# Kernel tuning notes

Measured on AMD Instinct MI355X. Metric: run time of the kernel, lower is better.

The kernel has to match this reference:

```python
import jax, jax.numpy as jnp
from jax import lax
import numpy as np

B, D = 1_000_000, 20


def setup_inputs() -> dict:
    key = jax.random.key(0)
    kx, kw, kb, ki = jax.random.split(key, 4)
    bound = 1.0 / np.sqrt(D)  # torch nn.Linear init scale
    return {
        "X": jax.random.normal(kx, (B, D), dtype=jnp.float32),
        "W": jax.random.uniform(kw, (D, D), dtype=jnp.float32, minval=-bound, maxval=bound),
        "b": jax.random.uniform(kb, (D,), dtype=jnp.float32, minval=-bound, maxval=bound),
        "W_init": jax.random.normal(ki, (D, D), dtype=jnp.float32),
    }


def reference(X, W, b, W_init):
    # linear -> matmul(+1) -> relu -> same linear again
    h = X @ W.T + b                       # [B, D]
    h = jax.nn.relu(h @ W_init + 1.0)     # [B, D]
    h = h @ W.T + b                       # [B, D]

    # while h.abs().sum() > 1: h /= 2
    # Halving by 2 is exact in fp32, so the abs-sum exactly halves each
    # iteration; count iterations on a scalar, then apply one fused scale.
    s0 = jnp.sum(jnp.abs(h))

    def cond(state):
        s, _ = state
        return s > 1.0

    def body(state):
        s, k = state
        return s * 0.5, k + 1

    _, k = lax.while_loop(cond, body, (s0, jnp.int32(0)))
    scale = jnp.exp2(-k.astype(h.dtype))  # 2**-k, exact for integer k
    return jnp.sum(h * scale)
```

## Files before the change

kernel.cpp:

```cpp
#include <hip/hip_runtime.h>
#include <math.h>

#define D 20
#define ITER 5

typedef __attribute__((ext_vector_type(8))) __bf16 bf16x8;
typedef __attribute__((ext_vector_type(4))) float f32x4;

#define WS_B1_BYTE 0
#define WS_B2_BYTE 2048
#define WS_C_BYTE 4096
#define WS_BB_BYTE 4224
#define WS_PART_BYTE 8192

__device__ __forceinline__ unsigned f2bf_u(float f) {
  unsigned u = __float_as_uint(f);
  u += 0x7fffu + ((u >> 16) & 1u);
  return u >> 16;
}

__global__ void prep_kernel(const float* __restrict__ W,
                            const float* __restrict__ b,
                            const float* __restrict__ Wi,
                            unsigned char* __restrict__ ws) {
  unsigned short* fb1 = (unsigned short*)(ws + WS_B1_BYTE);
  unsigned short* fb2 = (unsigned short*)(ws + WS_B2_BYTE);
  float* cpad = (float*)(ws + WS_C_BYTE);
  float* bpad = (float*)(ws + WS_BB_BYTE);

  const int t = threadIdx.x;
  {
    const int tile = t >> 9, rem = t & 511;
    const int lane = rem >> 3, j = rem & 7;
    const int k = (lane >> 4) * 8 + j;
    const int n = tile * 16 + (lane & 15);
    float v1 = 0.f, v2 = 0.f;
    if (k < D && n < D) {
      float a = 0.f;
#pragma unroll
      for (int e = 0; e < D; ++e) a = fmaf(W[e * D + k], Wi[e * D + n], a);
      v1 = a;
      v2 = W[n * D + k];
    }
    fb1[t] = (unsigned short)f2bf_u(v1);
    fb2[t] = (unsigned short)f2bf_u(v2);
  }
  if (t < 32) {
    float cv = 0.f, bv = 0.f;
    if (t < D) {
      float a = 1.0f;
#pragma unroll
      for (int e = 0; e < D; ++e) a = fmaf(b[e], Wi[e * D + t], a);
      cv = a;
      bv = b[t];
    }
    cpad[t] = cv;
    bpad[t] = bv;
  }
}

__global__ __launch_bounds__(256, 4) void fused_kernel(
    const float* __restrict__ X,
    const unsigned char* __restrict__ ws,
    double* __restrict__ partials) {
  __shared__ __align__(16) float sP[4 * 16 * 36];
  __shared__ float sred[8];

  const uint4* __restrict__ fb1 = (const uint4*)(ws + WS_B1_BYTE);
  const uint4* __restrict__ fb2 = (const uint4*)(ws + WS_B2_BYTE);
  const float* __restrict__ cpad = (const float*)(ws + WS_C_BYTE);
  const float* __restrict__ bpad = (const float*)(ws + WS_BB_BYTE);

  const int t = threadIdx.x;
  const int wave = t >> 6, lane = t & 63;
  const int m = lane & 15, oct = lane >> 4;
  const int k0 = oct * 8;
  const int ko1 = (k0 < D) ? k0 : 0;
  const int ko2 = (k0 + 4 < D) ? k0 + 4 : 0;
  const float s1m = (k0 < D) ? 1.f : 0.f;
  const float s2m = (k0 + 4 < D) ? 1.f : 0.f;

  union UB { bf16x8 v; uint4 q; } b10, b11, b20, b21;
  b10.q = fb1[0 * 64 + lane];
  b11.q = fb1[1 * 64 + lane];
  b20.q = fb2[0 * 64 + lane];
  b21.q = fb2[1 * 64 + lane];
  const float c0 = cpad[m], c1 = cpad[16 + m];
  const float bb0 = bpad[m], bb1 = bpad[16 + m];

  float* wp = sP + wave * 576;
  const float4* rp = (const float4*)(wp + m * 36 + k0);

  const long long wavebase = (long long)blockIdx.x * (4 * ITER * 16) + wave * (ITER * 16);

  float rs = 0.f, ra = 0.f;

  long long rowg = wavebase + m;
  float4 v1 = *(const float4*)(X + rowg * D + ko1);
  float4 v2 = *(const float4*)(X + rowg * D + ko2);

#pragma unroll
  for (int it = 0; it < ITER; ++it) {
    float4 n1, n2;
    if (it + 1 < ITER) {
      const long long rn = wavebase + (it + 1) * 16 + m;
      n1 = *(const float4*)(X + rn * D + ko1);
      n2 = *(const float4*)(X + rn * D + ko2);
    }

    union UF { bf16x8 v; unsigned u[4]; } a1;
    a1.u[0] = f2bf_u(v1.x * s1m) | (f2bf_u(v1.y * s1m) << 16);
    a1.u[1] = f2bf_u(v1.z * s1m) | (f2bf_u(v1.w * s1m) << 16);
    a1.u[2] = f2bf_u(v2.x * s2m) | (f2bf_u(v2.y * s2m) << 16);
    a1.u[3] = f2bf_u(v2.z * s2m) | (f2bf_u(v2.w * s2m) << 16);

    f32x4 acc0 = {c0, c0, c0, c0};
    f32x4 acc1 = {c1, c1, c1, c1};
    acc0 = __builtin_amdgcn_mfma_f32_16x16x32_bf16(a1.v, b10.v, acc0, 0, 0, 0);
    acc1 = __builtin_amdgcn_mfma_f32_16x16x32_bf16(a1.v, b11.v, acc1, 0, 0, 0);

#pragma unroll
    for (int i = 0; i < 4; ++i) {
      wp[(4 * oct + i) * 36 + m] = fmaxf(acc0[i], 0.f);
      wp[(4 * oct + i) * 36 + 16 + m] = fmaxf(acc1[i], 0.f);
    }
    float4 p1 = rp[0], p2 = rp[1];

    union UF a2;
    a2.u[0] = f2bf_u(p1.x) | (f2bf_u(p1.y) << 16);
    a2.u[1] = f2bf_u(p1.z) | (f2bf_u(p1.w) << 16);
    a2.u[2] = f2bf_u(p2.x) | (f2bf_u(p2.y) << 16);
    a2.u[3] = f2bf_u(p2.z) | (f2bf_u(p2.w) << 16);

    f32x4 d0 = {bb0, bb0, bb0, bb0};
    f32x4 d1 = {bb1, bb1, bb1, bb1};
    d0 = __builtin_amdgcn_mfma_f32_16x16x32_bf16(a2.v, b20.v, d0, 0, 0, 0);
    d1 = __builtin_amdgcn_mfma_f32_16x16x32_bf16(a2.v, b21.v, d1, 0, 0, 0);

#pragma unroll
    for (int i = 0; i < 4; ++i) {
      rs += d0[i] + d1[i];
      ra += fabsf(d0[i]) + fabsf(d1[i]);
    }

    if (it + 1 < ITER) {
      v1 = n1;
      v2 = n2;
    }
  }

#pragma unroll
  for (int off = 32; off > 0; off >>= 1) {
    rs += __shfl_down(rs, off, 64);
    ra += __shfl_down(ra, off, 64);
  }
  if (lane == 0) {
    sred[wave] = rs;
    sred[4 + wave] = ra;
  }
  __syncthreads();
  if (t == 0) {
    float s1 = sred[0] + sred[1] + sred[2] + sred[3];
    float s2 = sred[4] + sred[5] + sred[6] + sred[7];
    partials[2 * blockIdx.x + 0] = (double)s1;
    partials[2 * blockIdx.x + 1] = (double)s2;
  }
}

__global__ void fin_kernel(const double* __restrict__ partials,
                           float* __restrict__ out, int nblocks) {
  __shared__ double sredh[16], sreda[16];
  const int t = threadIdx.x;
  double sh = 0.0, sa = 0.0;
  for (int i = t; i < nblocks; i += 1024) {
    sh += partials[2 * i + 0];
    sa += partials[2 * i + 1];
  }
#pragma unroll
  for (int off = 32; off > 0; off >>= 1) {
    sh += __shfl_down(sh, off, 64);
    sa += __shfl_down(sa, off, 64);
  }
  const int wave = t >> 6, lane = t & 63;
  if (lane == 0) {
    sredh[wave] = sh;
    sreda[wave] = sa;
  }
  __syncthreads();
  if (t == 0) {
    double th = 0.0, ta = 0.0;
#pragma unroll
    for (int w = 0; w < 16; ++w) {
      th += sredh[w];
      ta += sreda[w];
    }
    int k = 0;
    while (ta > 1.0 && k < 1100) {
      ta *= 0.5;
      ++k;
    }
    out[0] = ldexpf((float)th, -k);
  }
}

extern "C" void kernel_launch(void* const* d_in, const int* in_sizes, int n_in,
                              void* d_out, int out_size, void* d_ws, size_t ws_size,
                              hipStream_t stream) {
  const float* X = (const float*)d_in[0];
  const float* W = (const float*)d_in[1];
  const float* b = (const float*)d_in[2];
  const float* Wi = (const float*)d_in[3];
  float* out = (float*)d_out;
  unsigned char* ws = (unsigned char*)d_ws;

  const int nrows = in_sizes[0] / D;
  const int nblocks = nrows / (4 * ITER * 16);
  double* partials = (double*)(ws + WS_PART_BYTE);

  hipLaunchKernelGGL(prep_kernel, dim3(1), dim3(1024), 0, stream, W, b, Wi, ws);
  hipLaunchKernelGGL(fused_kernel, dim3(nblocks), dim3(256), 0, stream,
                     X, ws, partials);
  hipLaunchKernelGGL(fin_kernel, dim3(1), dim3(1024), 0, stream, partials, out,
                     nblocks);
}
```

Measured before the change: 119.2 us.

## Fuse final reduction into main kernel via last-block atomic counter; use vector bf16 convert

Removes the separate finalize kernel launch. Each block now bumps an atomic counter after writing its partials, and the last block to finish reduces all partials and computes the output scale. Separately, the manual round-to-nearest bf16 packing is replaced with __builtin_convertvector, which can map to hardware packed conversion, and zero-padding is now done with bitmasks. This saves one launch and its gap, in exchange for a serial tail in the last block and an extra atomic and fence per block.

```diff
diff --git a/kernel.cpp b/kernel.cpp
--- a/kernel.cpp
+++ b/kernel.cpp
@@ -5,12 +5,14 @@
 #define ITER 5
 
 typedef __attribute__((ext_vector_type(8))) __bf16 bf16x8;
+typedef __attribute__((ext_vector_type(8))) float f32x8;
 typedef __attribute__((ext_vector_type(4))) float f32x4;
 
 #define WS_B1_BYTE 0
 #define WS_B2_BYTE 2048
 #define WS_C_BYTE 4096
 #define WS_BB_BYTE 4224
+#define WS_CNT_BYTE 4480
 #define WS_PART_BYTE 8192
 
 __device__ __forceinline__ unsigned f2bf_u(float f) {
@@ -29,6 +31,7 @@
   float* bpad = (float*)(ws + WS_BB_BYTE);
 
   const int t = threadIdx.x;
+  if (t == 0) *(unsigned*)(ws + WS_CNT_BYTE) = 0u;
   {
     const int tile = t >> 9, rem = t & 511;
     const int lane = rem >> 3, j = rem & 7;
@@ -62,9 +65,13 @@
 __global__ __launch_bounds__(256, 4) void fused_kernel(
     const float* __restrict__ X,
     const unsigned char* __restrict__ ws,
-    double* __restrict__ partials) {
+    double* __restrict__ partials,
+    unsigned* __restrict__ cnt,
+    float* __restrict__ out) {
   __shared__ __align__(16) float sP[4 * 16 * 36];
   __shared__ float sred[8];
+  __shared__ double sredh[4], sreda[4];
+  __shared__ int slast;
 
   const uint4* __restrict__ fb1 = (const uint4*)(ws + WS_B1_BYTE);
   const uint4* __restrict__ fb2 = (const uint4*)(ws + WS_B2_BYTE);
@@ -77,8 +84,8 @@
   const int k0 = oct * 8;
   const int ko1 = (k0 < D) ? k0 : 0;
   const int ko2 = (k0 + 4 < D) ? k0 + 4 : 0;
-  const float s1m = (k0 < D) ? 1.f : 0.f;
-  const float s2m = (k0 + 4 < D) ? 1.f : 0.f;
+  const unsigned msk1 = (k0 < D) ? 0xffffffffu : 0u;
+  const unsigned msk2 = (k0 + 4 < D) ? 0xffffffffu : 0u;
 
   union UB { bf16x8 v; uint4 q; } b10, b11, b20, b21;
   b10.q = fb1[0 * 64 + lane];
@@ -109,10 +116,14 @@
     }
 
     union UF { bf16x8 v; unsigned u[4]; } a1;
-    a1.u[0] = f2bf_u(v1.x * s1m) | (f2bf_u(v1.y * s1m) << 16);
-    a1.u[1] = f2bf_u(v1.z * s1m) | (f2bf_u(v1.w * s1m) << 16);
-    a1.u[2] = f2bf_u(v2.x * s2m) | (f2bf_u(v2.y * s2m) << 16);
-    a1.u[3] = f2bf_u(v2.z * s2m) | (f2bf_u(v2.w * s2m) << 16);
+    {
+      f32x8 f1 = {v1.x, v1.y, v1.z, v1.w, v2.x, v2.y, v2.z, v2.w};
+      a1.v = __builtin_convertvector(f1, bf16x8);
+      a1.u[0] &= msk1;
+      a1.u[1] &= msk1;
+      a1.u[2] &= msk2;
+      a1.u[3] &= msk2;
+    }
 
     f32x4 acc0 = {c0, c0, c0, c0};
     f32x4 acc1 = {c1, c1, c1, c1};
@@ -127,10 +138,10 @@
     float4 p1 = rp[0], p2 = rp[1];
 
     union UF a2;
-    a2.u[0] = f2bf_u(p1.x) | (f2bf_u(p1.y) << 16);
-    a2.u[1] = f2bf_u(p1.z) | (f2bf_u(p1.w) << 16);
-    a2.u[2] = f2bf_u(p2.x) | (f2bf_u(p2.y) << 16);
-    a2.u[3] = f2bf_u(p2.z) | (f2bf_u(p2.w) << 16);
+    {
+      f32x8 f2 = {p1.x, p1.y, p1.z, p1.w, p2.x, p2.y, p2.z, p2.w};
+      a2.v = __builtin_convertvector(f2, bf16x8);
+    }
 
     f32x4 d0 = {bb0, bb0, bb0, bb0};
     f32x4 d1 = {bb1, bb1, bb1, bb1};
@@ -162,44 +173,42 @@
   if (t == 0) {
     float s1 = sred[0] + sred[1] + sred[2] + sred[3];
     float s2 = sred[4] + sred[5] + sred[6] + sred[7];
-    partials[2 * blockIdx.x + 0] = (double)s1;
-    partials[2 * blockIdx.x + 1] = (double)s2;
-  }
-}
-
-__global__ void fin_kernel(const double* __restrict__ partials,
-                           float* __restrict__ out, int nblocks) {
-  __shared__ double sredh[16], sreda[16];
-  const int t = threadIdx.x;
-  double sh = 0.0, sa = 0.0;
-  for (int i = t; i < nblocks; i += 1024) {
-    sh += partials[2 * i + 0];
-    sa += partials[2 * i + 1];
-  }
-#pragma unroll
-  for (int off = 32; off > 0; off >>= 1) {
-    sh += __shfl_down(sh, off, 64);
-    sa += __shfl_down(sa, off, 64);
-  }
-  const int wave = t >> 6, lane = t & 63;
-  if (lane == 0) {
-    sredh[wave] = sh;
-    sreda[wave] = sa;
+    partials[2 * (long long)blockIdx.x + 0] = (double)s1;
+    partials[2 * (long long)blockIdx.x + 1] = (double)s2;
+    __threadfence();
+    unsigned old = atomicAdd(cnt, 1u);
+    slast = (old == gridDim.x - 1u) ? 1 : 0;
   }
   __syncthreads();
-  if (t == 0) {
-    double th = 0.0, ta = 0.0;
-#pragma unroll
-    for (int w = 0; w < 16; ++w) {
-      th += sredh[w];
-      ta += sreda[w];
-    }
-    int k = 0;
-    while (ta > 1.0 && k < 1100) {
-      ta *= 0.5;
-      ++k;
-    }
-    out[0] = ldexpf((float)th, -k);
+
+  if (slast) {
+    __threadfence();
+    const int nb = (int)gridDim.x;
+    double sh = 0.0, sa = 0.0;
+    for (int i = t; i < nb; i += 256) {
+      sh += partials[2 * i + 0];
+      sa += partials[2 * i + 1];
+    }
+#pragma unroll
+    for (int off = 32; off > 0; off >>= 1) {
+      sh += __shfl_down(sh, off, 64);
+      sa += __shfl_down(sa, off, 64);
+    }
+    if (lane == 0) {
+      sredh[wave] = sh;
+      sreda[wave] = sa;
+    }
+    __syncthreads();
+    if (t == 0) {
+      double th = sredh[0] + sredh[1] + sredh[2] + sredh[3];
+      double ta = sreda[0] + sreda[1] + sreda[2] + sreda[3];
+      int k = 0;
+      while (ta > 1.0 && k < 1100) {
+        ta *= 0.5;
+        ++k;
+      }
+      out[0] = ldexpf((float)th, -k);
+    }
   }
 }
 
@@ -216,10 +225,9 @@
   const int nrows = in_sizes[0] / D;
   const int nblocks = nrows / (4 * ITER * 16);
   double* partials = (double*)(ws + WS_PART_BYTE);
+  unsigned* cnt = (unsigned*)(ws + WS_CNT_BYTE);
 
   hipLaunchKernelGGL(prep_kernel, dim3(1), dim3(1024), 0, stream, W, b, Wi, ws);
   hipLaunchKernelGGL(fused_kernel, dim3(nblocks), dim3(256), 0, stream,
-                     X, ws, partials);
-  hipLaunchKernelGGL(fin_kernel, dim3(1), dim3(1024), 0, stream, partials, out,
-                     nblocks);
-}
+                     X, ws, partials, cnt, out);
+}
```

Result: slower. 237.5 us (+99.2%).
